# Performance work log

Hardware: AMD Instinct MI355X
Metric: run time of the kernel (lower is better)

## Reference

```python
import jax, jax.numpy as jnp
import numpy as np

B, T, D_IN, H, G = 64, 512, 862, 1024, 4096  # G = 4*H, PyTorch gate order i,f,g,o


def setup_inputs() -> dict:
    key = jax.random.key(0)
    ks = jax.random.split(key, 9)
    s0 = 1.0 / np.sqrt(H)  # PyTorch LSTM init scale
    return {
        "x": jax.random.normal(ks[0], (B, T, D_IN), dtype=jnp.float32),
        "W_ih0": jax.random.normal(ks[1], (G, D_IN), dtype=jnp.float32) * s0,
        "W_hh0": jax.random.normal(ks[2], (G, H), dtype=jnp.float32) * s0,
        "b_ih0": jax.random.normal(ks[3], (G,), dtype=jnp.float32) * s0,
        "b_hh0": jax.random.normal(ks[4], (G,), dtype=jnp.float32) * s0,
        "W_ih1": jax.random.normal(ks[5], (G, H), dtype=jnp.float32) * s0,
        "W_hh1": jax.random.normal(ks[6], (G, H), dtype=jnp.float32) * s0,
        "b_ih1": jax.random.normal(ks[7], (G,), dtype=jnp.float32) * s0,
        "b_hh1": jax.random.normal(ks[8], (G,), dtype=jnp.float32) * s0,
    }


def _lstm_layer(x, W_ih, W_hh, b_ih, b_hh):
    # x: [B, T, D]; gates precomputed for the input projection (one big GEMM)
    b, t, _ = x.shape
    h_dim = W_hh.shape[1]
    xg = jnp.einsum("btd,gd->btg", x, W_ih) + (b_ih + b_hh)  # [B, T, 4H]

    def step(carry, xt):
        h, c = carry
        g = xt + h @ W_hh.T  # [B, 4H]
        i, f, gc, o = jnp.split(g, 4, axis=-1)  # PyTorch order i,f,g,o
        i = jax.nn.sigmoid(i)
        f = jax.nn.sigmoid(f)
        gc = jnp.tanh(gc)
        o = jax.nn.sigmoid(o)
        c = f * c + i * gc
        h = o * jnp.tanh(c)
        return (h, c), h

    h0 = jnp.zeros((b, h_dim), x.dtype)
    c0 = jnp.zeros((b, h_dim), x.dtype)
    _, hs = jax.lax.scan(step, (h0, c0), jnp.swapaxes(xg, 0, 1))  # [T, B, H]
    return jnp.swapaxes(hs, 0, 1)  # [B, T, H]


def reference(x, W_ih0, W_hh0, b_ih0, b_hh0, W_ih1, W_hh1, b_ih1, b_hh1):
    h1 = _lstm_layer(x, W_ih0, W_hh0, b_ih0, b_hh0)
    out = _lstm_layer(h1, W_ih1, W_hh1, b_ih1, b_hh1)
    return out
```

## Files before the change

kernel.cpp:

```cpp
#include <hip/hip_runtime.h>
#include <cstdint>

#define BATCH 64
#define SEQ   512
#define DIN   862
#define DPAD  896
#define HID   1024
#define NG    4096
#define POIS  0xFFFFFFFFu

typedef _Float16 f16;
typedef __attribute__((ext_vector_type(8))) _Float16 f16x8;
typedef __attribute__((ext_vector_type(4))) float    f32x4;
typedef unsigned long long u64;

__device__ __forceinline__ void glds16(const f16* g, f16* l) {
    auto gp = (const __attribute__((address_space(1))) void*)(uintptr_t)g;
    auto lp = (__attribute__((address_space(3))) void*)(uint32_t)(uintptr_t)l;
    __builtin_amdgcn_global_load_lds(gp, lp, 16, 0, 0);
}

__device__ __forceinline__ float sigf(float x) {
    return __builtin_amdgcn_rcpf(1.f + __expf(-x));
}
__device__ __forceinline__ float tanh_fast(float x) {
    float xx = fminf(15.f, fmaxf(-15.f, x));
    float e = __expf(2.f * xx);
    return (e - 1.f) * __builtin_amdgcn_rcpf(e + 1.f);
}

__device__ __forceinline__ long xg_index(int t, int b, int n) {
    int bs = b >> 4, bl = b & 15;
    int g = n >> 10, jh = n & 1023;
    int jg = jh >> 4, jl = jh & 15;
    return (((((long)t * 4 + bs) * 64 + jg) * 4 + g) * 16 + bl) * 16 + jl;
}

__global__ __launch_bounds__(256) void prep_kernel(
    const float* __restrict__ x,
    const float* __restrict__ Wih0, const float* __restrict__ Whh0,
    const float* __restrict__ bih0, const float* __restrict__ bhh0,
    const float* __restrict__ Wih1, const float* __restrict__ Whh1,
    const float* __restrict__ bih1, const float* __restrict__ bhh1,
    f16* __restrict__ xh, f16* __restrict__ W0h, f16* __restrict__ Wh0h,
    f16* __restrict__ W1h, f16* __restrict__ Wh1h,
    float* __restrict__ b0, float* __restrict__ b1,
    unsigned* __restrict__ h1p, unsigned* __restrict__ h2p)
{
    long tid = (long)blockIdx.x * blockDim.x + threadIdx.x;
    long np  = (long)gridDim.x * blockDim.x;
    for (long i = tid; i < (long)BATCH * SEQ * DPAD; i += np) {
        long m = i / DPAD, k = i % DPAD;
        xh[i] = (k < DIN) ? (f16)x[m * DIN + k] : (f16)0.f;
    }
    for (long i = tid; i < (long)NG * DPAD; i += np) {
        long n = i / DPAD, k = i % DPAD;
        W0h[i] = (k < DIN) ? (f16)Wih0[n * DIN + k] : (f16)0.f;
    }
    for (long i = tid; i < (long)NG * HID; i += np) {
        Wh0h[i] = (f16)Whh0[i];
        W1h[i]  = (f16)Wih1[i];
        Wh1h[i] = (f16)Whh1[i];
    }
    for (long i = tid; i < NG; i += np) { b0[i] = bih0[i] + bhh0[i]; b1[i] = bih1[i] + bhh1[i]; }
    const long HW = (long)SEQ * BATCH * HID / 2;
    for (long i = tid; i < HW; i += np) {
        __hip_atomic_store(&h1p[i], POIS, __ATOMIC_RELAXED, __HIP_MEMORY_SCOPE_AGENT);
        __hip_atomic_store(&h2p[i], POIS, __ATOMIC_RELAXED, __HIP_MEMORY_SCOPE_AGENT);
    }
}

__global__ __launch_bounds__(256) void gemm_f16(
    const f16* __restrict__ A, const f16* __restrict__ Bw,
    const float* __restrict__ bias, f16* __restrict__ out, int K, int mode)
{
    __shared__ f16 smem[2 * 128 * 32];
    const int tid  = threadIdx.x;
    const int lane = tid & 63, wave = tid >> 6;
    const int wm = wave >> 1, wn = wave & 1;
    const int quad = lane >> 4, l15 = lane & 15;
    const int bm = blockIdx.x >> 5, bn = blockIdx.x & 31;
    const long m0 = (long)bm * 128, n0 = (long)bn * 128;
    const int r4 = lane >> 2, g4 = lane & 3;

    f32x4 acc[4][4];
#pragma unroll
    for (int i = 0; i < 4; ++i)
#pragma unroll
        for (int j = 0; j < 4; ++j)
#pragma unroll
            for (int r = 0; r < 4; ++r) acc[i][j][r] = 0.f;

#pragma unroll 1
    for (int kk = 0; kk < K; kk += 32) {
#pragma unroll
        for (int c = 0; c < 2; ++c) {
            int idx = wave * 2 + c;
            int lr  = idx * 16 + r4;
            int gs  = g4 ^ ((lr >> 1) & 3);
            glds16(A  + (m0 + lr) * (long)K + kk + gs * 8, smem + idx * 512);
            glds16(Bw + (n0 + lr) * (long)K + kk + gs * 8, smem + 4096 + idx * 512);
        }
        __syncthreads();
        f16x8 af[4], bf[4];
#pragma unroll
        for (int i = 0; i < 4; ++i) {
            int lr = 64 * wm + 16 * i + l15;
            int sl = quad ^ ((lr >> 1) & 3);
            af[i] = *(const f16x8*)(smem + lr * 32 + sl * 8);
        }
#pragma unroll
        for (int j = 0; j < 4; ++j) {
            int lr = 64 * wn + 16 * j + l15;
            int sl = quad ^ ((lr >> 1) & 3);
            bf[j] = *(const f16x8*)(smem + 4096 + lr * 32 + sl * 8);
        }
#pragma unroll
        for (int i = 0; i < 4; ++i)
#pragma unroll
            for (int j = 0; j < 4; ++j)
                acc[i][j] = __builtin_amdgcn_mfma_f32_16x16x32_f16(af[i], bf[j], acc[i][j], 0, 0, 0);
        __syncthreads();
    }

#pragma unroll
    for (int j = 0; j < 4; ++j) {
        int n = (int)n0 + 64 * wn + 16 * j + l15;
        float bv = bias[n];
#pragma unroll
        for (int i = 0; i < 4; ++i) {
#pragma unroll
            for (int r = 0; r < 4; ++r) {
                int m = (int)m0 + 64 * wm + 16 * i + quad * 4 + r;
                int t, b;
                if (mode == 1) { b = m >> 9; t = m & 511; }
                else           { t = m >> 6; b = m & 63; }
                out[xg_index(t, b, n)] = (f16)(acc[i][j][r] + bv);
            }
        }
    }
}

__global__ __launch_bounds__(256, 1) void lstm_layer(
    const f16* __restrict__ xg, const f16* __restrict__ Whh,
    f16* __restrict__ hseq, float* __restrict__ out32)
{
    __shared__ float P[4 * 4 * 16 * 17];
    const int tid = threadIdx.x;
    const int lane = tid & 63, w = tid >> 6;
    const int quad = lane >> 4, l15 = lane & 15;
    const int bs = blockIdx.x & 3;
    const int jg = blockIdx.x >> 2;
    const int ks0 = 256 * w;

    f16x8 wf[4][8];
#pragma unroll
    for (int g = 0; g < 4; ++g) {
        const f16* Wp = Whh + ((long)g * HID + jg * 16 + l15) * HID + ks0 + quad * 8;
#pragma unroll
        for (int s = 0; s < 8; ++s)
            wf[g][s] = *(const f16x8*)(Wp + s * 32);
    }
#pragma unroll
    for (int g = 0; g < 4; ++g)
#pragma unroll
        for (int s = 0; s < 8; ++s)
            asm volatile("" : "+v"(wf[g][s]));

    const int gb = tid >> 4, gj = tid & 15;
    const int bG = bs * 16 + gb, jG = jg * 16 + gj;
    unsigned* hw = (unsigned*)hseq;
    float cst = 0.f;

#pragma unroll 1
    for (int t = 0; t < SEQ; ++t) {
        const f16* xp = xg + (((long)t * 4 + bs) * 64 + jg) * 1024 + gb * 16 + gj;
        float xgi = (float)xp[0];
        float xgf = (float)xp[256];
        float xgg = (float)xp[512];
        float xgo = (float)xp[768];

        f32x4 acc[4];
#pragma unroll
        for (int g = 0; g < 4; ++g)
#pragma unroll
            for (int r = 0; r < 4; ++r) acc[g][r] = 0.f;

        if (t > 0) {
            const f16* hpf = hseq + ((long)(t - 1) * BATCH + bs * 16 + l15) * HID + ks0 + quad * 8;
            f16x8 af[8];
            for (;;) {
                bool ok = true;
#pragma unroll
                for (int s = 0; s < 8; ++s) {
                    const u64* p = (const u64*)(hpf + s * 32);
                    u64 a = __hip_atomic_load((u64*)p,
                                              __ATOMIC_RELAXED, __HIP_MEMORY_SCOPE_AGENT);
                    u64 b = __hip_atomic_load((u64*)p + 1,
                                              __ATOMIC_RELAXED, __HIP_MEMORY_SCOPE_AGENT);
                    ok = ok && ((unsigned)a != POIS) && ((unsigned)(a >> 32) != POIS)
                            && ((unsigned)b != POIS) && ((unsigned)(b >> 32) != POIS);
                    union { u64 u[2]; f16x8 v; } cv2;
                    cv2.u[0] = a; cv2.u[1] = b;
                    af[s] = cv2.v;
                }
                if (__all((int)ok)) break;
                __builtin_amdgcn_s_sleep(1);
            }
#pragma unroll
            for (int s = 0; s < 8; ++s)
#pragma unroll
                for (int g = 0; g < 4; ++g)
                    acc[g] = __builtin_amdgcn_mfma_f32_16x16x32_f16(af[s], wf[g][s], acc[g], 0, 0, 0);
        }

#pragma unroll
        for (int g = 0; g < 4; ++g)
#pragma unroll
            for (int r = 0; r < 4; ++r)
                P[((w * 4 + g) * 16 + quad * 4 + r) * 17 + l15] = acc[g][r];
        __syncthreads();

        float gate[4];
#pragma unroll
        for (int g = 0; g < 4; ++g) {
            float s0 = P[((0 * 4 + g) * 16 + gb) * 17 + gj];
            float s1 = P[((1 * 4 + g) * 16 + gb) * 17 + gj];
            float s2 = P[((2 * 4 + g) * 16 + gb) * 17 + gj];
            float s3 = P[((3 * 4 + g) * 16 + gb) * 17 + gj];
            gate[g] = (s0 + s1) + (s2 + s3);
        }
        __syncthreads();

        float gi = gate[0] + xgi;
        float gf = gate[1] + xgf;
        float gg = gate[2] + xgg;
        float go = gate[3] + xgo;
        float si = sigf(gi), sf = sigf(gf), so = sigf(go);
        float tg = tanh_fast(gg);
        cst = sf * cst + si * tg;
        float h = so * tanh_fast(cst);

        union { f16 f; unsigned short u; } cv; cv.f = (f16)h;
        unsigned hv = cv.u;
        unsigned ov = __shfl_xor(hv, 1);
        if (!(tid & 1))
            __hip_atomic_store(&hw[(((long)t * BATCH + bG) * HID + jG) >> 1],
                               hv | (ov << 16), __ATOMIC_RELAXED, __HIP_MEMORY_SCOPE_AGENT);
        if (out32) out32[((long)bG * SEQ + t) * HID + jG] = h;
    }
}

extern "C" void kernel_launch(void* const* d_in, const int* in_sizes, int n_in,
                              void* d_out, int out_size, void* d_ws, size_t ws_size,
                              hipStream_t stream) {
    (void)in_sizes; (void)n_in; (void)out_size; (void)ws_size;
    const float* x    = (const float*)d_in[0];
    const float* Wih0 = (const float*)d_in[1];
    const float* Whh0 = (const float*)d_in[2];
    const float* bih0 = (const float*)d_in[3];
    const float* bhh0 = (const float*)d_in[4];
    const float* Wih1 = (const float*)d_in[5];
    const float* Whh1 = (const float*)d_in[6];
    const float* bih1 = (const float*)d_in[7];
    const float* bhh1 = (const float*)d_in[8];

    char* ws = (char*)d_ws;
    size_t off = 0;
    auto alloc = [&](size_t bytes) { char* p = ws + off; off += (bytes + 255) & ~(size_t)255; return p; };
    f16*   XG   = (f16*)alloc((size_t)SEQ * BATCH * NG * 2);
    f16*   xh   = (f16*)alloc((size_t)BATCH * SEQ * DPAD * 2);
    f16*   h1   = (f16*)alloc((size_t)SEQ * BATCH * HID * 2);
    f16*   h2   = (f16*)alloc((size_t)SEQ * BATCH * HID * 2);
    f16*   W0h  = (f16*)alloc((size_t)NG * DPAD * 2);
    f16*   Wh0h = (f16*)alloc((size_t)NG * HID * 2);
    f16*   W1h  = (f16*)alloc((size_t)NG * HID * 2);
    f16*   Wh1h = (f16*)alloc((size_t)NG * HID * 2);
    float* b0   = (float*)alloc((size_t)NG * 4);
    float* b1   = (float*)alloc((size_t)NG * 4);

    prep_kernel<<<dim3(2048), dim3(256), 0, stream>>>(x, Wih0, Whh0, bih0, bhh0,
                                                      Wih1, Whh1, bih1, bhh1,
                                                      xh, W0h, Wh0h, W1h, Wh1h, b0, b1,
                                                      (unsigned*)h1, (unsigned*)h2);

    gemm_f16<<<dim3(8192), dim3(256), 0, stream>>>(xh, W0h, b0, XG, DPAD, 1);

    {
        const f16* xgp = XG; const f16* whp = Wh0h; f16* hp = h1; float* op = nullptr;
        void* args[] = { (void*)&xgp, (void*)&whp, (void*)&hp, (void*)&op };
        (void)hipLaunchCooperativeKernel((const void*)lstm_layer, dim3(256), dim3(256), args, 0, stream);
    }

    gemm_f16<<<dim3(8192), dim3(256), 0, stream>>>(h1, W1h, b1, XG, HID, 2);

    {
        const f16* xgp = XG; const f16* whp = Wh1h; f16* hp = h2; float* op = (float*)d_out;
        void* args[] = { (void*)&xgp, (void*)&whp, (void*)&hp, (void*)&op };
        (void)hipLaunchCooperativeKernel((const void*)lstm_layer, dim3(256), dim3(256), args, 0, stream);
    }
}
```

Before: 6.428 ms.

## Split LSTM recurrence across 512 blocks with 8-row batch groups and cached polling

Adds a recurrent kernel that splits each 16-row batch slice into two 8-row groups, so 512 persistent blocks run at two blocks per CU instead of 256 blocks at one. Polling for the previous hidden state now uses plain sc0 vector loads with a periodic agent-scope atomic reload, which cuts the latency of each poll. Hidden-state stores are issued at both workgroup and agent scope. The trade-off is duplicated weight fragments in registers across twice as many blocks, MFMA rows half-wasted on the 8-row groups, and reliance on sc0 loads eventually observing other CUs' writes.

```diff
diff --git a/kernel.cpp b/kernel.cpp
--- a/kernel.cpp
+++ b/kernel.cpp
@@ -34,6 +34,43 @@
     int g = n >> 10, jh = n & 1023;
     int jg = jh >> 4, jl = jh & 15;
     return (((((long)t * 4 + bs) * 64 + jg) * 4 + g) * 16 + bl) * 16 + jl;
+}
+
+__device__ __forceinline__ void load8_sc0(const f16* p, f16x8* af) {
+    asm volatile(
+        "global_load_dwordx4 %0, %8, off sc0\n\t"
+        "global_load_dwordx4 %1, %8, off offset:64 sc0\n\t"
+        "global_load_dwordx4 %2, %8, off offset:128 sc0\n\t"
+        "global_load_dwordx4 %3, %8, off offset:192 sc0\n\t"
+        "global_load_dwordx4 %4, %8, off offset:256 sc0\n\t"
+        "global_load_dwordx4 %5, %8, off offset:320 sc0\n\t"
+        "global_load_dwordx4 %6, %8, off offset:384 sc0\n\t"
+        "global_load_dwordx4 %7, %8, off offset:448 sc0\n\t"
+        "s_waitcnt vmcnt(0)"
+        : "=&v"(af[0]), "=&v"(af[1]), "=&v"(af[2]), "=&v"(af[3]),
+          "=&v"(af[4]), "=&v"(af[5]), "=&v"(af[6]), "=&v"(af[7])
+        : "v"(p)
+        : "memory");
+}
+__device__ __forceinline__ void load8_sc1(const f16* p, f16x8* af) {
+#pragma unroll
+    for (int s = 0; s < 8; ++s) {
+        const u64* q = (const u64*)(p + s * 32);
+        union { u64 u[2]; f16x8 v; } cv2;
+        cv2.u[0] = __hip_atomic_load((u64*)q,     __ATOMIC_RELAXED, __HIP_MEMORY_SCOPE_AGENT);
+        cv2.u[1] = __hip_atomic_load((u64*)q + 1, __ATOMIC_RELAXED, __HIP_MEMORY_SCOPE_AGENT);
+        af[s] = cv2.v;
+    }
+}
+__device__ __forceinline__ bool frags_ok(const f16x8* af) {
+    bool ok = true;
+#pragma unroll
+    for (int s = 0; s < 8; ++s) {
+        union { f16x8 v; unsigned u[4]; } c; c.v = af[s];
+#pragma unroll
+        for (int q = 0; q < 4; ++q) ok = ok && (c.u[q] != POIS);
+    }
+    return ok;
 }
 
 __global__ __launch_bounds__(256) void prep_kernel(
@@ -141,6 +178,121 @@
     }
 }
 
+__global__ __launch_bounds__(256, 2) void lstm_layer_x(
+    const f16* __restrict__ xg, const f16* __restrict__ Whh,
+    f16* __restrict__ hseq, float* __restrict__ out32)
+{
+    __shared__ float P[4 * 4 * 16 * 17];
+    const int tid = threadIdx.x;
+    const int lane = tid & 63, w = tid >> 6;
+    const int quad = lane >> 4, l15 = lane & 15;
+    const int grp = blockIdx.x & 7;
+    const int jg  = blockIdx.x >> 3;
+    const int ks0 = 256 * w;
+
+    __builtin_amdgcn_fence(__ATOMIC_ACQUIRE, "agent");
+
+    f16x8 wf[4][8];
+#pragma unroll
+    for (int g = 0; g < 4; ++g) {
+        const f16* Wp = Whh + ((long)g * HID + jg * 16 + l15) * HID + ks0 + quad * 8;
+#pragma unroll
+        for (int s = 0; s < 8; ++s)
+            wf[g][s] = *(const f16x8*)(Wp + s * 32);
+    }
+#pragma unroll
+    for (int g = 0; g < 4; ++g)
+#pragma unroll
+        for (int s = 0; s < 8; ++s)
+            asm volatile("" : "+v"(wf[g][s]));
+
+    const int gb = tid >> 4, gj = tid & 15;
+    const int bG = grp * 8 + gb;
+    const int jG = jg * 16 + gj;
+    unsigned* hw = (unsigned*)hseq;
+    float cst = 0.f;
+
+#pragma unroll 1
+    for (int t = 0; t < SEQ; ++t) {
+        float xgi = 0.f, xgf = 0.f, xgg = 0.f, xgo = 0.f;
+        if (tid < 128) {
+            int bs = bG >> 4, bl = bG & 15;
+            const f16* xp = xg + ((((long)t * 4 + bs) * 64 + jg) * 4) * 256 + bl * 16 + gj;
+            xgi = (float)xp[0];
+            xgf = (float)xp[256];
+            xgg = (float)xp[512];
+            xgo = (float)xp[768];
+        }
+
+        f32x4 acc[4];
+#pragma unroll
+        for (int g = 0; g < 4; ++g)
+#pragma unroll
+            for (int r = 0; r < 4; ++r) acc[g][r] = 0.f;
+
+        if (t > 0) {
+            const f16* hpf = hseq + ((long)(t - 1) * BATCH + grp * 8 + (l15 & 7)) * HID
+                                  + ks0 + quad * 8;
+            f16x8 af[8];
+            int it = 0;
+            for (;;) {
+                if ((it & 7) != 7) load8_sc0(hpf, af);
+                else               load8_sc1(hpf, af);
+                ++it;
+                if (__all((int)frags_ok(af))) break;
+                __builtin_amdgcn_s_sleep(1);
+            }
+#pragma unroll
+            for (int s = 0; s < 8; ++s)
+#pragma unroll
+                for (int g = 0; g < 4; ++g)
+                    acc[g] = __builtin_amdgcn_mfma_f32_16x16x32_f16(af[s], wf[g][s], acc[g], 0, 0, 0);
+        }
+
+#pragma unroll
+        for (int g = 0; g < 4; ++g)
+#pragma unroll
+            for (int r = 0; r < 4; ++r)
+                P[((w * 4 + g) * 16 + quad * 4 + r) * 17 + l15] = acc[g][r];
+        __syncthreads();
+
+        float gate[4] = {0.f, 0.f, 0.f, 0.f};
+        if (tid < 128) {
+#pragma unroll
+            for (int g = 0; g < 4; ++g) {
+                float s0 = P[((0 * 4 + g) * 16 + gb) * 17 + gj];
+                float s1 = P[((1 * 4 + g) * 16 + gb) * 17 + gj];
+                float s2 = P[((2 * 4 + g) * 16 + gb) * 17 + gj];
+                float s3 = P[((3 * 4 + g) * 16 + gb) * 17 + gj];
+                gate[g] = (s0 + s1) + (s2 + s3);
+            }
+        }
+        __syncthreads();
+
+        if (tid < 128) {
+            float gi = gate[0] + xgi;
+            float gf = gate[1] + xgf;
+            float gg = gate[2] + xgg;
+            float go = gate[3] + xgo;
+            float si = sigf(gi), sf = sigf(gf), so = sigf(go);
+            float tg = tanh_fast(gg);
+            cst = sf * cst + si * tg;
+            float h = so * tanh_fast(cst);
+
+            union { f16 f; unsigned short u; } cv; cv.f = (f16)h;
+            unsigned hv = cv.u;
+            unsigned ov = __shfl_xor(hv, 1);
+            if (!(tid & 1)) {
+                unsigned val = hv | (ov << 16);
+                unsigned* p = &hw[(((long)t * BATCH + bG) * HID + jG) >> 1];
+                __hip_atomic_store(p, val, __ATOMIC_RELAXED, __HIP_MEMORY_SCOPE_WORKGROUP);
+                __hip_atomic_store(p, val, __ATOMIC_RELAXED, __HIP_MEMORY_SCOPE_AGENT);
+            }
+            if (out32) out32[((long)bG * SEQ + t) * HID + jG] = h;
+        }
+    }
+}
+
 __global__ __launch_bounds__(256, 1) void lstm_layer(
     const f16* __restrict__ xg, const f16* __restrict__ Whh,
     f16* __restrict__ hseq, float* __restrict__ out32)
@@ -190,21 +342,8 @@
             const f16* hpf = hseq + ((long)(t - 1) * BATCH + bs * 16 + l15) * HID + ks0 + quad * 8;
             f16x8 af[8];
             for (;;) {
-                bool ok = true;
-#pragma unroll
-                for (int s = 0; s < 8; ++s) {
-                    const u64* p = (const u64*)(hpf + s * 32);
-                    u64 a = __hip_atomic_load((u64*)p,
-                                              __ATOMIC_RELAXED, __HIP_MEMORY_SCOPE_AGENT);
-                    u64 b = __hip_atomic_load((u64*)p + 1,
-                                              __ATOMIC_RELAXED, __HIP_MEMORY_SCOPE_AGENT);
-                    ok = ok && ((unsigned)a != POIS) && ((unsigned)(a >> 32) != POIS)
-                            && ((unsigned)b != POIS) && ((unsigned)(b >> 32) != POIS);
-                    union { u64 u[2]; f16x8 v; } cv2;
-                    cv2.u[0] = a; cv2.u[1] = b;
-                    af[s] = cv2.v;
-                }
-                if (__all((int)ok)) break;
+                load8_sc1(hpf, af);
+                if (__all((int)frags_ok(af))) break;
                 __builtin_amdgcn_s_sleep(1);
             }
 #pragma unroll
@@ -286,10 +425,17 @@
 
     gemm_f16<<<dim3(8192), dim3(256), 0, stream>>>(xh, W0h, b0, XG, DPAD, 1);
 
+    int occ = 0;
+    (void)hipOccupancyMaxActiveBlocksPerMultiprocessor(&occ, (const void*)lstm_layer_x, 256, 0);
+    const bool use_x = (occ >= 2);
+
     {
         const f16* xgp = XG; const f16* whp = Wh0h; f16* hp = h1; float* op = nullptr;
         void* args[] = { (void*)&xgp, (void*)&whp, (void*)&hp, (void*)&op };
-        (void)hipLaunchCooperativeKernel((const void*)lstm_layer, dim3(256), dim3(256), args, 0, stream);
+        if (use_x)
+            (void)hipLaunchCooperativeKernel((const void*)lstm_layer_x, dim3(512), dim3(256), args, 0, stream);
+        else
+            (void)hipLaunchCooperativeKernel((const void*)lstm_layer, dim3(256), dim3(256), args, 0, stream);
     }
 
     gemm_f16<<<dim3(8192), dim3(256), 0, stream>>>(h1, W1h, b1, XG, HID, 2);
@@ -297,6 +443,9 @@
     {
         const f16* xgp = XG; const f16* whp = Wh1h; f16* hp = h2; float* op = (float*)d_out;
         void* args[] = { (void*)&xgp, (void*)&whp, (void*)&hp, (void*)&op };
-        (void)hipLaunchCooperativeKernel((const void*)lstm_layer, dim3(256), dim3(256), args, 0, stream);
-    }
-}
+        if (use_x)
+            (void)hipLaunchCooperativeKernel((const void*)lstm_layer_x, dim3(512), dim3(256), args, 0, stream);
+        else
+            (void)hipLaunchCooperativeKernel((const void*)lstm_layer, dim3(256), dim3(256), args, 0, stream);
+    }
+}
```

Result: faster. 6.266 ms (-2.5%).
